# Kernel optimization log

Hardware: AMD Instinct MI355X
Metric: run time of the kernel (lower is better)

Reference implementation:

```python
import jax, jax.numpy as jnp
import numpy as np

HEIGHT = 0.1        # height_factor
MIN_DIST = 10       # min_distance
PROM = 0.05         # prominence_factor


def _find_peaks(xn):
    """scipy.signal.find_peaks(xn, height=HEIGHT, distance=MIN_DIST,
    prominence=PROM) for a single 1D signal, vectorized.
    (Plateau handling omitted: for continuous random inputs exact ties have
    probability zero, so strict local maxima match scipy's _local_maxima_1d.)"""
    N = xn.shape[0]
    pos = jnp.arange(N)

    # 1) strict local maxima (endpoints can never be peaks in scipy)
    interior = (xn[1:-1] > xn[:-2]) & (xn[1:-1] > xn[2:])
    is_peak = jnp.pad(interior, (1, 1), constant_values=False)

    # 2) height filter
    cand = is_peak & (xn >= HEIGHT)

    # 3) distance-based greedy suppression: highest peak first, remove
    #    neighbors with |i-j| < MIN_DIST (matches _select_by_peak_distance)
    order = jnp.argsort(-xn)  # descending by value

    def step(suppressed, idx):
        keep_this = cand[idx] & ~suppressed[idx]
        near = (jnp.abs(pos - idx) < MIN_DIST) & (pos != idx)
        suppressed = suppressed | (keep_this & near)
        return suppressed, keep_this

    _, keeps = jax.lax.scan(step, jnp.zeros(N, dtype=bool), order)
    keep = jnp.zeros(N, dtype=bool).at[order].set(keeps)

    # 4) prominence (wlen=None -> full-signal base search, per position):
    #    left base  = min x over (L, i] where L = last j<i with x[j] > x[i]
    #    right base = min x over [i, R) where R = first j>i with x[j] > x[i]
    greater = xn[None, :] > xn[:, None]              # [i, j]: x_j > x_i
    left_stop = greater & (pos[None, :] < pos[:, None])
    L = jnp.max(jnp.where(left_stop, pos[None, :], -1), axis=1)
    right_stop = greater & (pos[None, :] > pos[:, None])
    R = jnp.min(jnp.where(right_stop, pos[None, :], N), axis=1)

    big = jnp.asarray(jnp.inf, xn.dtype)
    in_l = (pos[None, :] > L[:, None]) & (pos[None, :] <= pos[:, None])
    lmin = jnp.min(jnp.where(in_l, xn[None, :], big), axis=1)
    in_r = (pos[None, :] >= pos[:, None]) & (pos[None, :] < R[:, None])
    rmin = jnp.min(jnp.where(in_r, xn[None, :], big), axis=1)
    prominence = xn - jnp.maximum(lmin, rmin)

    keep = keep & (prominence >= PROM)
    return keep.astype(xn.dtype)


def setup_inputs() -> dict:
    key = jax.random.key(0)
    x = jax.random.normal(key, (16, 2048), dtype=jnp.float32)
    return {"x": x}


def reference(x):
    # per-sample min-max normalization, as in the torch module
    xmin = jnp.min(x, axis=-1, keepdims=True)
    xmax = jnp.max(x, axis=-1, keepdims=True)
    xn = (x - xmin) / (xmax - xmin + 1e-5)
    return jax.vmap(_find_peaks)(xn)
```

## Files before the change

### kernel.cpp

```cpp
#include <hip/hip_runtime.h>

#define N 2048
#define NT 256
#define EL 8
#define HEIGHTF 0.1f
#define PROMF 0.05f
#define MD1 9
#define LVLS 8

__global__ __launch_bounds__(NT)
void peak_kernel(const float* __restrict__ x, float* __restrict__ out) {
    __shared__ float xs[N];
    __shared__ float actl[16 + N + 24];
    __shared__ unsigned int nk32[3 + NT + 3];
    __shared__ float TMX[LVLS][N];
    __shared__ float TMN[LVLS][N];
    __shared__ float wred[8];
    __shared__ int cont[2];
    __shared__ int wtot[4];
    __shared__ unsigned short klist[NT];
    __shared__ unsigned char keepres[N];

    const int row = blockIdx.x;
    const int t = threadIdx.x;
    const int base = t * EL;
    const float* xr = x + row * (size_t)N;
    const int wv = t >> 6, ln = t & 63;

    float4 Ld0 = ((const float4*)(xr + base))[0];
    float4 Ld1 = ((const float4*)(xr + base))[1];
    float v0[EL] = {Ld0.x, Ld0.y, Ld0.z, Ld0.w, Ld1.x, Ld1.y, Ld1.z, Ld1.w};
    float mn = v0[0], mx = v0[0];
    #pragma unroll
    for (int e = 1; e < EL; ++e) { mn = fminf(mn, v0[e]); mx = fmaxf(mx, v0[e]); }
    #pragma unroll
    for (int off = 32; off > 0; off >>= 1) {
        mn = fminf(mn, __shfl_xor(mn, off, 64));
        mx = fmaxf(mx, __shfl_xor(mx, off, 64));
    }
    if (ln == 0) { wred[wv] = mn; wred[4 + wv] = mx; }
    if (t == 0) {
        nk32[0] = 0; nk32[1] = 0; nk32[2] = 0;
        nk32[3+NT] = 0; nk32[3+NT+1] = 0; nk32[3+NT+2] = 0;
        cont[0] = 0;
    }
    if (t < 16) actl[t] = -1e30f;
    if (t < 24) actl[16 + N + t] = -1e30f;
    __syncthreads();

    const float xmin = fminf(fminf(wred[0], wred[1]), fminf(wred[2], wred[3]));
    const float xmax = fmaxf(fmaxf(wred[4], wred[5]), fmaxf(wred[6], wred[7]));
    const float den = (xmax - xmin) + 1e-5f;
    float vn[EL];
    #pragma unroll
    for (int e = 0; e < EL; ++e) {
        vn[e] = (v0[e] - xmin) / den;
        xs[base + e] = vn[e];
    }
    __syncthreads();

    unsigned int undec = 0, kept = 0;
    #pragma unroll
    for (int e = 0; e < EL; ++e) {
        int i = base + e;
        float v = vn[e];
        float lf = (e == 0) ? ((i >= 1) ? xs[i-1] : 3e38f) : vn[e-1];
        float rt = (e == EL-1) ? ((i+1 < N) ? xs[i+1] : 3e38f) : vn[e+1];
        bool c = (i >= 1) && (i <= N-2) && (v > lf) && (v > rt) && (v >= HEIGHTF);
        if (c) undec |= (1u << e);
        actl[16 + i] = c ? v : -1e30f;
    }
    __syncthreads();

    float a[40];
    {
        const float4* ap = (const float4*)(actl + base);
        #pragma unroll
        for (int q = 0; q < 10; ++q) {
            float4 w = ap[q];
            a[4*q+0] = w.x; a[4*q+1] = w.y; a[4*q+2] = w.z; a[4*q+3] = w.w;
        }
    }

    auto compute_wins = [&](unsigned int ud) -> unsigned int {
        float m2v[25], m4v[23], m8v[19];
        #pragma unroll
        for (int s = 0; s < 25; ++s) m2v[s] = fmaxf(a[7+s], a[8+s]);
        #pragma unroll
        for (int s = 0; s < 23; ++s) m4v[s] = fmaxf(m2v[s], m2v[s+2]);
        #pragma unroll
        for (int s = 0; s < 19; ++s) m8v[s] = fmaxf(m4v[s], m4v[s+4]);
        unsigned int wb = 0;
        #pragma unroll
        for (int e = 0; e < EL; ++e) {
            if (ud & (1u << e)) {
                float v = a[16+e];
                float wl = fmaxf(m8v[e], a[15+e]);
                float wr = fmaxf(m8v[10+e], a[25+e]);
                if (wl < v && wr <= v) wb |= (1u << e);
            }
        }
        return wb;
    };

    unsigned int winb = undec ? compute_wins(undec) : 0u;

    unsigned int* nkp = nk32 + 3;
    for (int round = 0; round < 2048; ++round) {
        nkp[t] = winb;
        if (t == 0) cont[(round + 1) & 1] = 0;
        if (undec) cont[round & 1] = 1;
        __syncthreads();
        if (cont[round & 1] == 0) break;
        unsigned long long V = 0;
        #pragma unroll
        for (int q = 0; q < 7; ++q)
            V |= ((unsigned long long)(nkp[t - 3 + q] & 0xFFu)) << (8 * q);
        V <<= 1;
        if (__ballot(V != 0ULL)) {
            #pragma unroll
            for (int e = 0; e < EL; ++e) {
                if (undec & (1u << e)) {
                    unsigned int w19 = (unsigned int)((V >> (16 + e)) & 0x7FFFFULL);
                    if (w19 & (1u << 9)) { kept |= (1u << e); undec &= ~(1u << e); }
                    else if (w19)        { undec &= ~(1u << e); }
                }
            }
            #pragma unroll
            for (int s = 0; s < 40; ++s) {
                if ((V >> s) & 0x7FFFFULL) a[s] = -1e30f;
            }
        }
        winb = 0;
        if (__ballot(undec != 0)) winb = compute_wins(undec);
    }

    float cx[EL], cn[EL];
    #pragma unroll
    for (int j = 0; j < EL; ++j) {
        int i = t + j * NT;
        float a0 = xs[i];
        bool inb = (i + 1 < N);
        float nb = inb ? xs[i + 1] : 0.0f;
        cx[j] = fmaxf(a0, inb ? nb : -3e38f);
        cn[j] = fminf(a0, inb ? nb : 3e38f);
        TMX[0][i] = cx[j];
        TMN[0][i] = cn[j];
    }
    int myc = __popc(kept);
    int pre = myc;
    #pragma unroll
    for (int off = 1; off < 64; off <<= 1) {
        int up = __shfl_up(pre, off, 64);
        if (ln >= off) pre += up;
    }
    if (ln == 63) wtot[wv] = pre;
    #pragma unroll
    for (int e = 0; e < EL; ++e) keepres[base + e] = 0;
    __syncthreads();

    {
        int woff = 0;
        #pragma unroll
        for (int w = 0; w < 4; ++w) woff += (w < wv) ? wtot[w] : 0;
        int slot = woff + pre - myc;
        #pragma unroll
        for (int e = 0; e < EL; ++e)
            if (kept & (1u << e)) klist[slot++] = (unsigned short)(base + e);
    }
    const int ktot = wtot[0] + wtot[1] + wtot[2] + wtot[3];
    for (int Lv = 1; Lv < LVLS; ++Lv) {
        int h = 1 << Lv;
        #pragma unroll
        for (int j = 0; j < EL; ++j) {
            int i = t + j * NT;
            bool inb = (i + h < N);
            float bx = inb ? TMX[Lv-1][i+h] : -3e38f;
            float bn = inb ? TMN[Lv-1][i+h] : 3e38f;
            cx[j] = fmaxf(cx[j], bx);
            cn[j] = fminf(cn[j], bn);
            TMX[Lv][i] = cx[j];
            TMN[Lv][i] = cn[j];
        }
        __syncthreads();
    }

    if (t < ktot) {
        const int i = klist[t];
        const float v = xs[i];
        float m = v;
        int p = i - 1;
        while (p >= 0) {
            int len = p + 1;
            int k = (len >= (1 << LVLS)) ? LVLS : (31 - __clz(len));
            int s = p + 1 - (1 << k);
            float wmx = (k == 0) ? xs[s] : TMX[k-1][s];
            if (wmx > v) {
                while (k > 0) {
                    int half = 1 << (k - 1);
                    int rs = s + half;
                    float rm = (k == 1) ? xs[rs] : TMX[k-2][rs];
                    if (rm > v) s = rs;
                    else m = fminf(m, (k == 1) ? xs[rs] : TMN[k-2][rs]);
                    --k;
                }
                break;
            } else {
                m = fminf(m, (k == 0) ? xs[s] : TMN[k-1][s]);
                p = s - 1;
            }
        }
        const float lmin = m;
        m = v;
        p = i + 1;
        while (p < N) {
            int len = N - p;
            int k = (len >= (1 << LVLS)) ? LVLS : (31 - __clz(len));
            float wmx = (k == 0) ? xs[p] : TMX[k-1][p];
            if (wmx > v) {
                while (k > 0) {
                    int half = 1 << (k - 1);
                    float lm = (k == 1) ? xs[p] : TMX[k-2][p];
                    if (!(lm > v)) {
                        m = fminf(m, (k == 1) ? xs[p] : TMN[k-2][p]);
                        p += half;
                    }
                    --k;
                }
                break;
            } else {
                m = fminf(m, (k == 0) ? xs[p] : TMN[k-1][p]);
                p += 1 << k;
            }
        }
        const float rmin = m;
        if (v - fmaxf(lmin, rmin) >= PROMF) keepres[i] = 1;
    }
    __syncthreads();

    float res[EL];
    #pragma unroll
    for (int e = 0; e < EL; ++e) res[e] = keepres[base + e] ? 1.0f : 0.0f;
    float* outr = out + row * (size_t)N + base;
    ((float4*)outr)[0] = make_float4(res[0], res[1], res[2], res[3]);
    ((float4*)outr)[1] = make_float4(res[4], res[5], res[6], res[7]);
}

extern "C" void kernel_launch(void* const* d_in, const int* in_sizes, int n_in,
                              void* d_out, int out_size, void* d_ws, size_t ws_size,
                              hipStream_t stream) {
    const float* x = (const float*)d_in[0];
    float* outp = (float*)d_out;
    const int rows = in_sizes[0] / N;
    peak_kernel<<<rows, NT, 0, stream>>>(x, outp);
}
```

Baseline: 24.26 us.

## Replace barrier-synchronized suppression rounds with spin-wait asynchronous resolution; fuse sparse-table levels

The greedy distance-suppression loop no longer uses a __syncthreads per round. Each thread polls its neighbours' kept bits through volatile shared memory, resolves its candidates on its own, and a shared done-counter with sleep-based polling decides when to exit. The sparse-table build now computes two levels per barrier, and the left and right prominence searches run interleaved in one loop for more memory-level parallelism. The goal is fewer block barriers; the cost is spin-wait overhead and a reliance on forward progress and memory visibility across waves, with a guard counter as a fallback.

```diff
diff --git a/kernel.cpp b/kernel.cpp
--- a/kernel.cpp
+++ b/kernel.cpp
@@ -5,7 +5,6 @@
 #define EL 8
 #define HEIGHTF 0.1f
 #define PROMF 0.05f
-#define MD1 9
 #define LVLS 8
 
 __global__ __launch_bounds__(NT)
@@ -16,10 +15,10 @@
     __shared__ float TMX[LVLS][N];
     __shared__ float TMN[LVLS][N];
     __shared__ float wred[8];
-    __shared__ int cont[2];
     __shared__ int wtot[4];
     __shared__ unsigned short klist[NT];
     __shared__ unsigned char keepres[N];
+    __shared__ int donecnt;
 
     const int row = blockIdx.x;
     const int t = threadIdx.x;
@@ -39,11 +38,9 @@
         mx = fmaxf(mx, __shfl_xor(mx, off, 64));
     }
     if (ln == 0) { wred[wv] = mn; wred[4 + wv] = mx; }
-    if (t == 0) {
-        nk32[0] = 0; nk32[1] = 0; nk32[2] = 0;
-        nk32[3+NT] = 0; nk32[3+NT+1] = 0; nk32[3+NT+2] = 0;
-        cont[0] = 0;
-    }
+    nk32[t] = 0;
+    if (t < 6) nk32[NT + t] = 0;
+    if (t == 0) donecnt = 0;
     if (t < 16) actl[t] = -1e30f;
     if (t < 24) actl[16 + N + t] = -1e30f;
     __syncthreads();
@@ -103,37 +100,52 @@
         return wb;
     };
 
-    unsigned int winb = undec ? compute_wins(undec) : 0u;
-
-    unsigned int* nkp = nk32 + 3;
-    for (int round = 0; round < 2048; ++round) {
-        nkp[t] = winb;
-        if (t == 0) cont[(round + 1) & 1] = 0;
-        if (undec) cont[round & 1] = 1;
-        __syncthreads();
-        if (cont[round & 1] == 0) break;
-        unsigned long long V = 0;
-        #pragma unroll
-        for (int q = 0; q < 7; ++q)
-            V |= ((unsigned long long)(nkp[t - 3 + q] & 0xFFu)) << (8 * q);
-        V <<= 1;
-        if (__ballot(V != 0ULL)) {
-            #pragma unroll
-            for (int e = 0; e < EL; ++e) {
-                if (undec & (1u << e)) {
-                    unsigned int w19 = (unsigned int)((V >> (16 + e)) & 0x7FFFFULL);
-                    if (w19 & (1u << 9)) { kept |= (1u << e); undec &= ~(1u << e); }
-                    else if (w19)        { undec &= ~(1u << e); }
+    {
+        volatile unsigned int* nkv = nk32 + 3;
+        volatile int* dcp = (volatile int*)&donecnt;
+        unsigned long long lastV = ~0ULL;
+        bool counted = false;
+        int guard = 0;
+        while (true) {
+            if (undec) {
+                unsigned long long V = 0;
+                #pragma unroll
+                for (int q = 0; q < 7; ++q)
+                    V |= ((unsigned long long)(nkv[t - 3 + q] & 0xFFu)) << (8 * q);
+                V <<= 1;
+                if (V != lastV) {
+                    lastV = V;
+                    #pragma unroll
+                    for (int s = 0; s < 40; ++s)
+                        if ((V >> s) & 0x7FFFFULL) a[s] = -1e30f;
+                    #pragma unroll
+                    for (int e = 0; e < EL; ++e)
+                        if (undec & (1u << e))
+                            if ((V >> (16 + e)) & 0x7FFFFULL) undec &= ~(1u << e);
+                    if (undec) {
+                        unsigned int wb = compute_wins(undec);
+                        if (wb) {
+                            kept |= wb;
+                            undec = 0;
+                            nkv[t] = kept;
+                        }
+                    }
+                } else {
+                    __builtin_amdgcn_s_sleep(1);
                 }
             }
-            #pragma unroll
-            for (int s = 0; s < 40; ++s) {
-                if ((V >> s) & 0x7FFFFULL) a[s] = -1e30f;
-            }
-        }
-        winb = 0;
-        if (__ballot(undec != 0)) winb = compute_wins(undec);
-    }
+            if (!undec && !counted) {
+                nkv[t] = kept;
+                __threadfence_block();
+                atomicAdd(&donecnt, 1);
+                counted = true;
+            }
+            if (*dcp >= NT) break;
+            if (counted) __builtin_amdgcn_s_sleep(2);
+            if (++guard > 65536) break;
+        }
+    }
+    __syncthreads();
 
     float cx[EL], cn[EL];
     #pragma unroll
@@ -169,18 +181,37 @@
             if (kept & (1u << e)) klist[slot++] = (unsigned short)(base + e);
     }
     const int ktot = wtot[0] + wtot[1] + wtot[2] + wtot[3];
-    for (int Lv = 1; Lv < LVLS; ++Lv) {
-        int h = 1 << Lv;
+    #pragma unroll
+    for (int pp = 0; pp < 3; ++pp) {
+        const int Lv = 1 + 2 * pp;
+        const int h = 1 << Lv;
         #pragma unroll
         for (int j = 0; j < EL; ++j) {
             int i = t + j * NT;
-            bool inb = (i + h < N);
-            float bx = inb ? TMX[Lv-1][i+h] : -3e38f;
-            float bn = inb ? TMN[Lv-1][i+h] : 3e38f;
-            cx[j] = fmaxf(cx[j], bx);
-            cn[j] = fminf(cn[j], bn);
-            TMX[Lv][i] = cx[j];
-            TMN[Lv][i] = cn[j];
+            float x1 = (i +   h < N) ? TMX[Lv-1][i+  h] : -3e38f;
+            float x2 = (i + 2*h < N) ? TMX[Lv-1][i+2*h] : -3e38f;
+            float x3 = (i + 3*h < N) ? TMX[Lv-1][i+3*h] : -3e38f;
+            float n1 = (i +   h < N) ? TMN[Lv-1][i+  h] : 3e38f;
+            float n2 = (i + 2*h < N) ? TMN[Lv-1][i+2*h] : 3e38f;
+            float n3 = (i + 3*h < N) ? TMN[Lv-1][i+3*h] : 3e38f;
+            float tx = fmaxf(cx[j], x1), tn = fminf(cn[j], n1);
+            TMX[Lv][i] = tx;  TMN[Lv][i] = tn;
+            cx[j] = fmaxf(tx, fmaxf(x2, x3));
+            cn[j] = fminf(tn, fminf(n2, n3));
+            TMX[Lv+1][i] = cx[j];  TMN[Lv+1][i] = cn[j];
+        }
+        __syncthreads();
+    }
+    {
+        const int h = 128;
+        #pragma unroll
+        for (int j = 0; j < EL; ++j) {
+            int i = t + j * NT;
+            float x1 = (i + h < N) ? TMX[6][i+h] : -3e38f;
+            float n1 = (i + h < N) ? TMN[6][i+h] : 3e38f;
+            cx[j] = fmaxf(cx[j], x1);
+            cn[j] = fminf(cn[j], n1);
+            TMX[7][i] = cx[j];  TMN[7][i] = cn[j];
         }
         __syncthreads();
     }
@@ -188,53 +219,59 @@
     if (t < ktot) {
         const int i = klist[t];
         const float v = xs[i];
-        float m = v;
-        int p = i - 1;
-        while (p >= 0) {
-            int len = p + 1;
-            int k = (len >= (1 << LVLS)) ? LVLS : (31 - __clz(len));
-            int s = p + 1 - (1 << k);
-            float wmx = (k == 0) ? xs[s] : TMX[k-1][s];
-            if (wmx > v) {
-                while (k > 0) {
-                    int half = 1 << (k - 1);
-                    int rs = s + half;
-                    float rm = (k == 1) ? xs[rs] : TMX[k-2][rs];
-                    if (rm > v) s = rs;
-                    else m = fminf(m, (k == 1) ? xs[rs] : TMN[k-2][rs]);
-                    --k;
-                }
-                break;
-            } else {
-                m = fminf(m, (k == 0) ? xs[s] : TMN[k-1][s]);
-                p = s - 1;
-            }
-        }
-        const float lmin = m;
-        m = v;
-        p = i + 1;
-        while (p < N) {
-            int len = N - p;
-            int k = (len >= (1 << LVLS)) ? LVLS : (31 - __clz(len));
-            float wmx = (k == 0) ? xs[p] : TMX[k-1][p];
-            if (wmx > v) {
-                while (k > 0) {
-                    int half = 1 << (k - 1);
-                    float lm = (k == 1) ? xs[p] : TMX[k-2][p];
-                    if (!(lm > v)) {
-                        m = fminf(m, (k == 1) ? xs[p] : TMN[k-2][p]);
-                        p += half;
-                    }
-                    --k;
-                }
-                break;
-            } else {
-                m = fminf(m, (k == 0) ? xs[p] : TMN[k-1][p]);
-                p += 1 << k;
-            }
-        }
-        const float rmin = m;
-        if (v - fmaxf(lmin, rmin) >= PROMF) keepres[i] = 1;
+        const float* TX0 = &TMX[0][0];
+        const float* TN0 = &TMN[0][0];
+        int Lph = 0, Lp = i - 1, Lk = 0, Ls = 0;
+        float Lm = v;
+        if (Lp < 0) Lph = 2;
+        int Rph = 0, Rp = i + 1, Rk = 0;
+        float Rm = v;
+        if (Rp >= N) Rph = 2;
+        while (Lph != 2 || Rph != 2) {
+            int lLev = 0, lIdx = 0, rLev = 0, rIdx = 0, Lrs = 0;
+            if (Lph == 0) {
+                int len = Lp + 1;
+                Lk = (len >= (1 << LVLS)) ? LVLS : (31 - __clz(len));
+                Ls = Lp + 1 - (1 << Lk);
+                lLev = Lk - 1; lIdx = Ls;
+            } else if (Lph == 1) {
+                Lrs = Ls + (1 << (Lk - 1));
+                lLev = Lk - 2; lIdx = Lrs;
+            }
+            if (Rph == 0) {
+                int len = N - Rp;
+                Rk = (len >= (1 << LVLS)) ? LVLS : (31 - __clz(len));
+                rLev = Rk - 1; rIdx = Rp;
+            } else if (Rph == 1) {
+                rLev = Rk - 2; rIdx = Rp;
+            }
+            float lx = 0.0f, lnv = 0.0f, rx = 0.0f, rnv = 0.0f;
+            if (Lph != 2) {
+                const float* bX = (lLev < 0) ? xs : (TX0 + lLev * N);
+                const float* bN = (lLev < 0) ? xs : (TN0 + lLev * N);
+                lx = bX[lIdx]; lnv = bN[lIdx];
+            }
+            if (Rph != 2) {
+                const float* bX = (rLev < 0) ? xs : (TX0 + rLev * N);
+                const float* bN = (rLev < 0) ? xs : (TN0 + rLev * N);
+                rx = bX[rIdx]; rnv = bN[rIdx];
+            }
+            if (Lph == 0) {
+                if (lx > v) Lph = (Lk == 0) ? 2 : 1;
+                else { Lm = fminf(Lm, lnv); Lp = Ls - 1; if (Lp < 0) Lph = 2; }
+            } else if (Lph == 1) {
+                if (lx > v) Ls = Lrs; else Lm = fminf(Lm, lnv);
+                if (--Lk == 0) Lph = 2;
+            }
+            if (Rph == 0) {
+                if (rx > v) Rph = (Rk == 0) ? 2 : 1;
+                else { Rm = fminf(Rm, rnv); Rp += (1 << Rk); if (Rp >= N) Rph = 2; }
+            } else if (Rph == 1) {
+                if (!(rx > v)) { Rm = fminf(Rm, rnv); Rp += (1 << (Rk - 1)); }
+                if (--Rk == 0) Rph = 2;
+            }
+        }
+        if (v - fmaxf(Lm, Rm) >= PROMF) keepres[i] = 1;
     }
     __syncthreads();
 
```

After: 23.24 us. 1.04x faster.
